# Kernel tuning notes

Hardware: AMD Instinct MI355X
Metric: run time of the kernel (lower is better)

Reference implementation:

```python
import jax, jax.numpy as jnp
import numpy as np

HIDDEN = 1024
INTER = 4096
N_EXPERTS = 8


def geglu(x, w1, w2, w3):
    # x: [N, C], w1/w2: [C, I], w3: [I, C]
    return (jax.nn.gelu(x @ w1, approximate=False) * (x @ w2)) @ w3


def setup_inputs() -> dict:
    key = jax.random.key(0)
    ks = jax.random.split(key, 8)
    s = 0.02
    x = jax.random.normal(ks[0], (2, 2048, HIDDEN), dtype=jnp.float32)
    w1s = jax.random.normal(ks[1], (HIDDEN, INTER), dtype=jnp.float32) * s
    w2s = jax.random.normal(ks[2], (HIDDEN, INTER), dtype=jnp.float32) * s
    w3s = jax.random.normal(ks[3], (INTER, HIDDEN), dtype=jnp.float32) * s
    W1 = jax.random.normal(ks[4], (N_EXPERTS, HIDDEN, INTER), dtype=jnp.float32) * s
    W2 = jax.random.normal(ks[5], (N_EXPERTS, HIDDEN, INTER), dtype=jnp.float32) * s
    W3 = jax.random.normal(ks[6], (N_EXPERTS, INTER, HIDDEN), dtype=jnp.float32) * s
    Wg = jax.random.normal(ks[7], (HIDDEN, N_EXPERTS), dtype=jnp.float32) * s
    return {"x": x, "w1s": w1s, "w2s": w2s, "w3s": w3s,
            "W1": W1, "W2": W2, "W3": W3, "Wg": Wg}


def reference(x, w1s, w2s, w3s, W1, W2, W3, Wg):
    B, T, C = x.shape
    xf = x.reshape(-1, C)  # [N, C]
    shared = geglu(xf, w1s, w2s, w3s)  # [N, C]
    logits = xf @ Wg  # [N, E]
    # top-1 of softmax == argmax of logits (softmax is monotone);
    # NOTE: original torch code does NOT multiply by the routing prob.
    idx = jnp.argmax(logits, axis=-1)  # [N]
    final = jnp.zeros_like(xf)
    for e in range(N_EXPERTS):  # small fixed expert count
        y = geglu(xf, W1[e], W2[e], W3[e])  # [N, C]
        final = final + jnp.where((idx == e)[:, None], y, 0.0)
    return (shared + final).reshape(B, T, C)
```

## Files before the change

### kernel.cpp

```cpp
#include <hip/hip_runtime.h>
#include <stdint.h>

#define HIDDEN 1024
#define INTER  4096
#define NTOK   4096
#define HROWS  (2*NTOK)
#define MAXB   72
#define NMAT   27

typedef unsigned short u16;
typedef unsigned int   u32;
typedef __bf16  bf16x8 __attribute__((ext_vector_type(8)));
typedef float   f32x4  __attribute__((ext_vector_type(4)));
typedef u32     u32x4  __attribute__((ext_vector_type(4)));

#define WAITVM(N) asm volatile("s_waitcnt vmcnt(" #N ")" ::: "memory")

__device__ __forceinline__ void hard_barrier() {
  asm volatile("" ::: "memory");
  __builtin_amdgcn_s_barrier();
  asm volatile("" ::: "memory");
}

__device__ __forceinline__ u16 f2bf(float f) {
  u32 u = __float_as_uint(f);
  u32 r = u + 0x7FFFu + ((u >> 16) & 1u);
  return (u16)(r >> 16);
}

__device__ __forceinline__ u32 cvt_pk_bf16(float lo, float hi) {
  u32 r;
  asm("v_cvt_pk_bf16_f32 %0, %1, %2" : "=v"(r) : "v"(lo), "v"(hi));
  return r;
}

__device__ __forceinline__ void glds16(const void* g, void* l) {
  __builtin_amdgcn_global_load_lds(
      (const __attribute__((address_space(1))) void*)g,
      (__attribute__((address_space(3))) void*)l, 16, 0, 0);
}

__device__ __forceinline__ f32x4 ntload4(const float* p) {
  return __builtin_nontemporal_load((const f32x4*)p);
}

__device__ __forceinline__ int xcd_swz(int orig, int T) {
  int q = T >> 3, r = T & 7;
  int xcd = orig & 7, pos = orig >> 3;
  return (xcd < r ? xcd * (q + 1) : r * (q + 1) + (xcd - r) * q) + pos;
}

__device__ __forceinline__ void blk_entry(const int* cnts, int bx,
                                          int& g, int& hrow0, int& rows, int& pb) {
  if (bx < 32) { g = 8; hrow0 = bx * 128; rows = 128; pb = 0; return; }
  int b = bx - 32, o = 0; g = -1;
  #pragma unroll
  for (int e = 0; e < 8; ++e) {
    int ne = (cnts[e] + 127) >> 7;
    if (g < 0) {
      if (b < ne) {
        g = e; pb = o + b * 128;
        rows = cnts[e] - b * 128; if (rows > 128) rows = 128;
        hrow0 = NTOK + pb;
      } else b -= ne;
    }
    o += cnts[e];
  }
}


__global__ __launch_bounds__(256) void k_pre(
    const float* __restrict__ w1s, const float* __restrict__ w2s,
    const float* __restrict__ w3s, const float* __restrict__ W1,
    const float* __restrict__ W2,  const float* __restrict__ W3,
    u16* __restrict__ Wb,
    const float* __restrict__ x,   const float* __restrict__ wg,
    int* __restrict__ idx, int* __restrict__ cnt, u16* __restrict__ xb)
{
  __shared__ float tileF[32 * 256];
  int tid = threadIdx.x;

  if (blockIdx.x < NMAT * 512) {
    int bid = blockIdx.x;
    int m = bid >> 9, pair = bid & 511;
    const float* src; int N, nkt, kt, pp2;
    if (m < 18) {
      N = INTER; nkt = 32;
      int mm = (m < 9) ? m : m - 9;
      const float* sp = (m < 9) ? w1s : w2s;
      const float* ep = (m < 9) ? W1 : W2;
      src = (mm == 0) ? sp : ep + (size_t)(mm - 1) * HIDDEN * INTER;
      kt = pair >> 4; pp2 = pair & 15;
    } else {
      N = HIDDEN; nkt = 128;
      int mm = m - 18;
      src = (mm == 0) ? w3s : W3 + (size_t)(mm - 1) * INTER * HIDDEN;
      kt = pair >> 2; pp2 = pair & 3;
    }

    const float* in0 = src + (size_t)(kt * 32) * N + pp2 * 256;
    #pragma unroll
    for (int i = 0; i < 8; ++i) {
      int f = tid + 256 * i;
      int k = f >> 6, c4 = f & 63;
      *(f32x4*)&tileF[k * 256 + c4 * 4] = ntload4(in0 + (size_t)k * N + c4 * 4);
    }
    __syncthreads();

    int p2 = tid >> 7, n = tid & 127;
    int pidx = m * 1024 + (pp2 * 2 + p2) * nkt + kt;
    u16* outp = Wb + (size_t)pidx * 4096 + n * 32;
    #pragma unroll
    for (int s = 0; s < 4; ++s) {
      int k8 = s ^ ((n >> 1) & 3);
      const float* col = &tileF[(k8 * 8) * 256 + p2 * 128 + n];
      u32x4 pk;
      pk.x = cvt_pk_bf16(col[0],    col[256]);
      pk.y = cvt_pk_bf16(col[512],  col[768]);
      pk.z = cvt_pk_bf16(col[1024], col[1280]);
      pk.w = cvt_pk_bf16(col[1536], col[1792]);
      *(u32x4*)(outp + s * 8) = pk;
    }
  } else {
    int gb = blockIdx.x - NMAT * 512;
    int wave = tid >> 6, lane = tid & 63;
    int t = gb * 4 + wave;
    if (t >= NTOK) return;
    float acc[8];
    #pragma unroll
    for (int e = 0; e < 8; ++e) acc[e] = 0.f;
    const float* xr = x + (size_t)t * HIDDEN;
    u16* xbr = xb + (size_t)t * HIDDEN;
    #pragma unroll
    for (int it = 0; it < HIDDEN / 4 / 64; ++it) {
      int c4i = it * 64 + lane;
      f32x4 xv = *(const f32x4*)(xr + c4i * 4);
      ushort4 o;
      o.x = f2bf(xv.x); o.y = f2bf(xv.y); o.z = f2bf(xv.z); o.w = f2bf(xv.w);
      *(ushort4*)(xbr + c4i * 4) = o;
      const float* wr = wg + (size_t)c4i * 32;
      #pragma unroll
      for (int u = 0; u < 4; ++u)
        #pragma unroll
        for (int e = 0; e < 8; ++e) acc[e] += xv[u] * wr[u * 8 + e];
    }
    #pragma unroll
    for (int e = 0; e < 8; ++e)
      for (int s = 32; s; s >>= 1) acc[e] += __shfl_xor(acc[e], s);
    if (lane == 0) {
      int best = 0; float bv = acc[0];
      #pragma unroll
      for (int e = 1; e < 8; ++e) if (acc[e] > bv) { bv = acc[e]; best = e; }
      idx[t] = best;
      atomicAdd(&cnt[best], 1);
    }
  }
}

__global__ void k_scatter(const int* __restrict__ idx, const int* __restrict__ cnt,
                          int* __restrict__ fill, int* __restrict__ perm) {
  int t = blockIdx.x * blockDim.x + threadIdx.x;
  if (t >= NTOK) return;
  int e = idx[t];
  int off = 0;
  #pragma unroll
  for (int j = 0; j < 8; ++j) off += (j < e) ? cnt[j] : 0;
  int p = atomicAdd(&fill[e], 1);
  perm[off + p] = t;
}


#define M1_TILE(B, STG, WN)                                                          \
  do {                                                                               \
    const u16* LA = pAr  + (B) * 12288;                                              \
    const u16* L1 = pBr1 + (B) * 12288;                                              \
    const u16* L2 = pBr2 + (B) * 12288;                                              \
    if (STG) {                                                                       \
      char* Ld = smem + (((B) + 2) % 3) * 24576;                                     \
      glds16(srcA0, Ld + w * 2048);                                                  \
      glds16(srcA1, Ld + w * 2048 + 1024);                                           \
      glds16(srcB1, Ld + 8192 + w * 2048);                                           \
      glds16(srcB1 + 1024, Ld + 8192 + w * 2048 + 1024);                             \
      glds16(srcB2, Ld + 16384 + w * 2048);                                          \
      glds16(srcB2 + 1024, Ld + 16384 + w * 2048 + 1024);                            \
      srcA0 += 64; srcA1 += 64; srcB1 += 8192; srcB2 += 8192;                        \
    }                                                                                \
    bf16x8 af[4], b1[4], b2[4];                                                      \
    _Pragma("unroll")                                                                \
    for (int mi = 0; mi < 4; ++mi) af[mi] = *(const bf16x8*)(LA + mi * 512);         \
    _Pragma("unroll")                                                                \
    for (int ni = 0; ni < 4; ++ni) {                                                 \
      b1[ni] = *(const bf16x8*)(L1 + ni * 512);                                      \
      b2[ni] = *(const bf16x8*)(L2 + ni * 512);                                      \
    }                                                                                \
    __builtin_amdgcn_s_setprio(1);                                                   \
    _Pragma("unroll")                                                                \
    for (int mi = 0; mi < 4; ++mi)                                                   \
      _Pragma("unroll")                                                              \
      for (int ni = 0; ni < 4; ++ni) {                                               \
        acc1[mi][ni] = __builtin_amdgcn_mfma_f32_16x16x32_bf16(af[mi], b1[ni], acc1[mi][ni], 0, 0, 0); \
        acc2[mi][ni] = __builtin_amdgcn_mfma_f32_16x16x32_bf16(af[mi], b2[ni], acc2[mi][ni], 0, 0, 0); \
      }                                                                              \
    __builtin_amdgcn_s_setprio(0);                                                   \
    WN;                                                                              \
    hard_barrier();                                                                  \
  } while (0)

__global__ __launch_bounds__(256, 2) void k_mlp1(
    const u16* __restrict__ xb, const u16* __restrict__ Wb,
    const int* __restrict__ perm, const int* __restrict__ cnt,
    u16* __restrict__ Hbuf)
{
  int cnts[8];
  #pragma unroll
  for (int e = 0; e < 8; ++e) cnts[e] = cnt[e];
  int nb = 32;
  #pragma unroll
  for (int e = 0; e < 8; ++e) nb += (cnts[e] + 127) >> 7;
  int T = nb * 32;
  int lid = blockIdx.x;
  if (lid >= T) return;
  int virt = xcd_swz(lid, T);
  int pp = virt / nb;
  int bx = virt - pp * nb;

  int g, hrow0, rows, pb;
  blk_entry(cnts, bx, g, hrow0, rows, pb);
  int m1 = (g == 8) ? 0 : 1 + g;
  int nbase = pp * 128;

  extern __shared__ __align__(16) char smem[];
  int tid = threadIdx.x;
  int w = tid >> 6, lane = tid & 63;
  int q = lane >> 4, rl = lane & 15;
  int mw = w >> 1, nw = w & 1;

  int tokj[2];
  #pragma unroll
  for (int j = 0; j < 2; ++j) {
    int r = w * 32 + j * 16 + (lane >> 2);
    int rc = (r < rows) ? r : (rows - 1);
    tokj[j] = (g == 8) ? (hrow0 + rc) : perm[pb + rc];
  }
  int gch = ((lane & 3) ^ ((lane >> 3) & 3)) * 16;

  const char* srcA0 = (const char*)xb + (size_t)tokj[0] * 2048 + gch;
  const char* srcA1 = (const char*)xb + (size_t)tokj[1] * 2048 + gch;
  const char* srcB1 = (const char*)Wb + ((size_t)m1 * 1024 + pp * 32) * 8192 + w * 2048 + (lane << 4);
  const char* srcB2 = (const char*)Wb + ((size_t)(m1 + 9) * 1024 + pp * 32) * 8192 + w * 2048 + (lane << 4);

  int co = (q ^ ((rl >> 1) & 3)) * 8;
  const u16* pAr  = (const u16*)smem + (mw * 64 + rl) * 32 + co;
  const u16* pBr1 = (const u16*)smem + 4096 + (nw * 64 + rl) * 32 + co;
  const u16* pBr2 = (const u16*)smem + 8192 + (nw * 64 + rl) * 32 + co;

  f32x4 acc1[4][4], acc2[4][4];
  f32x4 z = {0.f, 0.f, 0.f, 0.f};
  #pragma unroll
  for (int mi = 0; mi < 4; ++mi)
    #pragma unroll
    for (int ni = 0; ni < 4; ++ni) { acc1[mi][ni] = z; acc2[mi][ni] = z; }

  #pragma unroll
  for (int p = 0; p < 2; ++p) {
    char* Ld = smem + p * 24576;
    glds16(srcA0, Ld + w * 2048);
    glds16(srcA1, Ld + w * 2048 + 1024);
    glds16(srcB1, Ld + 8192 + w * 2048);
    glds16(srcB1 + 1024, Ld + 8192 + w * 2048 + 1024);
    glds16(srcB2, Ld + 16384 + w * 2048);
    glds16(srcB2 + 1024, Ld + 16384 + w * 2048 + 1024);
    srcA0 += 64; srcA1 += 64; srcB1 += 8192; srcB2 += 8192;
  }
  WAITVM(6);
  hard_barrier();

  for (int r = 0; r < 10; ++r) {
    M1_TILE(0, 1, WAITVM(6));
    M1_TILE(1, 1, WAITVM(6));
    M1_TILE(2, 1, WAITVM(6));
  }
  M1_TILE(0, 0, WAITVM(0));
  M1_TILE(1, 0, (void)0);

  #pragma unroll
  for (int mi = 0; mi < 4; ++mi) {
    #pragma unroll
    for (int j = 0; j < 4; ++j) {
      int r = mw * 64 + mi * 16 + q * 4 + j;
      if (r < rows) {
        size_t hb = (size_t)(hrow0 + r) * INTER + nbase + nw * 64;
        #pragma unroll
        for (int ni = 0; ni < 4; ++ni) {
          float h1 = acc1[mi][ni][j];
          float h2 = acc2[mi][ni][j];
          float ge = 0.5f * h1 * (1.0f + erff(h1 * 0.7071067811865476f));
          __builtin_nontemporal_store(f2bf(ge * h2), &Hbuf[hb + ni * 16 + rl]);
        }
      }
    }
  }
}


#define M2_TILE(B, STG, WN)                                                          \
  do {                                                                               \
    const u16* LA = pAr + (B) * 8192;                                                \
    const u16* LB = pBr + (B) * 8192;                                                \
    if (STG) {                                                                       \
      char* Ld = smem + (((B) + 2) % 3) * 16384;                                     \
      glds16(srcA0, Ld + w * 2048);                                                  \
      glds16(srcA1, Ld + w * 2048 + 1024);                                           \
      glds16(srcB0, Ld + 8192 + w * 2048);                                           \
      glds16(srcB0 + 1024, Ld + 8192 + w * 2048 + 1024);                             \
      srcA0 += 64; srcA1 += 64; srcB0 += 8192;                                       \
    }                                                                                \
    bf16x8 af[4], bf[4];                                                             \
    _Pragma("unroll")                                                                \
    for (int mi = 0; mi < 4; ++mi) af[mi] = *(const bf16x8*)(LA + mi * 512);         \
    _Pragma("unroll")                                                                \
    for (int ni = 0; ni < 4; ++ni) bf[ni] = *(const bf16x8*)(LB + ni * 512);         \
    __builtin_amdgcn_s_setprio(1);                                                   \
    _Pragma("unroll")                                                                \
    for (int mi = 0; mi < 4; ++mi)                                                   \
      _Pragma("unroll")                                                              \
      for (int ni = 0; ni < 4; ++ni)                                                 \
        acc[mi][ni] = __builtin_amdgcn_mfma_f32_16x16x32_bf16(af[mi], bf[ni], acc[mi][ni], 0, 0, 0); \
    __builtin_amdgcn_s_setprio(0);                                                   \
    WN;                                                                              \
    hard_barrier();                                                                  \
  } while (0)

__global__ __launch_bounds__(256, 3) void k_mlp2(
    const u16* __restrict__ Hbuf, const u16* __restrict__ Wb,
    const int* __restrict__ perm, const int* __restrict__ cnt,
    float* __restrict__ out, float* __restrict__ yexp)
{
  int cnts[8];
  #pragma unroll
  for (int e = 0; e < 8; ++e) cnts[e] = cnt[e];
  int nb = 32;
  #pragma unroll
  for (int e = 0; e < 8; ++e) nb += (cnts[e] + 127) >> 7;
  int T = nb * 8;
  int lid = blockIdx.x;
  if (lid >= T) return;
  int virt = xcd_swz(lid, T);
  int pp = virt / nb;
  int bx = virt - pp * nb;

  int g, hrow0, rows, pb;
  blk_entry(cnts, bx, g, hrow0, rows, pb);
  int m3 = (g == 8) ? 18 : 19 + g;
  int nbase = pp * 128;

  extern __shared__ __align__(16) char smem[];
  int tid = threadIdx.x;
  int w = tid >> 6, lane = tid & 63;
  int q = lane >> 4, rl = lane & 15;
  int mw = w >> 1, nw = w & 1;

  int hr[2];
  #pragma unroll
  for (int j = 0; j < 2; ++j) {
    int r = w * 32 + j * 16 + (lane >> 2);
    int rc = (r < rows) ? r : (rows - 1);
    hr[j] = hrow0 + rc;
  }
  int gch = ((lane & 3) ^ ((lane >> 3) & 3)) * 16;

  const char* srcA0 = (const char*)Hbuf + (size_t)hr[0] * (INTER * 2) + gch;
  const char* srcA1 = (const char*)Hbuf + (size_t)hr[1] * (INTER * 2) + gch;
  const char* srcB0 = (const char*)Wb + ((size_t)m3 * 1024 + pp * 128) * 8192 + w * 2048 + (lane << 4);

  int co = (q ^ ((rl >> 1) & 3)) * 8;
  const u16* pAr = (const u16*)smem + (mw * 64 + rl) * 32 + co;
  const u16* pBr = (const u16*)smem + 4096 + (nw * 64 + rl) * 32 + co;

  f32x4 acc[4][4];
  f32x4 z = {0.f, 0.f, 0.f, 0.f};
  #pragma unroll
  for (int mi = 0; mi < 4; ++mi)
    #pragma unroll
    for (int ni = 0; ni < 4; ++ni) acc[mi][ni] = z;

  #pragma unroll
  for (int p = 0; p < 2; ++p) {
    char* Ld = smem + p * 16384;
    glds16(srcA0, Ld + w * 2048);
    glds16(srcA1, Ld + w * 2048 + 1024);
    glds16(srcB0, Ld + 8192 + w * 2048);
    glds16(srcB0 + 1024, Ld + 8192 + w * 2048 + 1024);
    srcA0 += 64; srcA1 += 64; srcB0 += 8192;
  }
  WAITVM(4);
  hard_barrier();

  for (int r = 0; r < 42; ++r) {
    M2_TILE(0, 1, WAITVM(4));
    M2_TILE(1, 1, WAITVM(4));
    M2_TILE(2, 1, WAITVM(4));
  }
  M2_TILE(0, 0, WAITVM(0));
  M2_TILE(1, 0, (void)0);

  float* dstb = (g == 8) ? out : yexp;
  #pragma unroll
  for (int mi = 0; mi < 4; ++mi) {
    #pragma unroll
    for (int j = 0; j < 4; ++j) {
      int r = mw * 64 + mi * 16 + q * 4 + j;
      if (r < rows) {
        int tok = (g == 8) ? (hrow0 + r) : perm[pb + r];
        size_t ob = (size_t)tok * HIDDEN + nbase + nw * 64;
        #pragma unroll
        for (int ni = 0; ni < 4; ++ni)
          __builtin_nontemporal_store(acc[mi][ni][j], &dstb[ob + ni * 16 + rl]);
      }
    }
  }
}

__global__ void k_add(float* __restrict__ out, const float* __restrict__ yexp, int n4) {
  int i = blockIdx.x * blockDim.x + threadIdx.x;
  if (i >= n4) return;
  f32x4 a = __builtin_nontemporal_load(&((const f32x4*)out)[i]);
  f32x4 b = __builtin_nontemporal_load(&((const f32x4*)yexp)[i]);
  a += b;
  ((f32x4*)out)[i] = a;
}


extern "C" void kernel_launch(void* const* d_in, const int* in_sizes, int n_in,
                              void* d_out, int out_size, void* d_ws, size_t ws_size,
                              hipStream_t stream) {
  const float* x   = (const float*)d_in[0];
  const float* w1s = (const float*)d_in[1];
  const float* w2s = (const float*)d_in[2];
  const float* w3s = (const float*)d_in[3];
  const float* W1  = (const float*)d_in[4];
  const float* W2  = (const float*)d_in[5];
  const float* W3  = (const float*)d_in[6];
  const float* Wg  = (const float*)d_in[7];
  float* out = (float*)d_out;

  char* ws = (char*)d_ws;
  size_t o_xb   = 0;
  size_t o_H    = o_xb   + (size_t)NTOK * HIDDEN * 2;
  size_t o_yexp = o_H    + (size_t)HROWS * INTER * 2;
  size_t o_Wb   = o_yexp + (size_t)NTOK * HIDDEN * 4;
  size_t o_idx  = o_Wb   + (size_t)NMAT * 1024 * 8192;
  size_t o_perm = o_idx  + (size_t)NTOK * 4;
  size_t o_cnt  = o_perm + (size_t)NTOK * 4;
  size_t o_fill = o_cnt  + 32;
  size_t need   = o_fill + 32;
  if (ws_size < need) return;

  u16*  xb   = (u16*)(ws + o_xb);
  u16*  Hbuf = (u16*)(ws + o_H);
  float* yexp = (float*)(ws + o_yexp);
  u16*  Wb   = (u16*)(ws + o_Wb);
  int*  idx  = (int*)(ws + o_idx);
  int*  perm = (int*)(ws + o_perm);
  int*  cnt  = (int*)(ws + o_cnt);
  int*  fill = (int*)(ws + o_fill);

  hipMemsetAsync(ws + o_cnt, 0, 64, stream);
  k_pre<<<NMAT * 512 + NTOK / 4, 256, 0, stream>>>(w1s, w2s, w3s, W1, W2, W3, Wb,
                                                   x, Wg, idx, cnt, xb);
  k_scatter<<<NTOK / 256, 256, 0, stream>>>(idx, cnt, fill, perm);
  k_mlp1<<<MAXB * 32, 256, 73728, stream>>>(xb, Wb, perm, cnt, Hbuf);
  k_mlp2<<<MAXB * 8, 256, 49152, stream>>>(Hbuf, Wb, perm, cnt, out, yexp);
  k_add<<<(NTOK * HIDDEN / 4) / 256, 256, 0, stream>>>(out, yexp, NTOK * HIDDEN / 4);
}
```

Before: 473.5 us.

## Fuse shared and expert down-projection into one accumulation, drop k_add and yexp

```diff
diff --git a/kernel.cpp b/kernel.cpp
--- a/kernel.cpp
+++ b/kernel.cpp
@@ -6,6 +6,7 @@
 #define NTOK   4096
 #define HROWS  (2*NTOK)
 #define MAXB   72
+#define MAXB2  40
 #define NMAT   27
 
 typedef unsigned short u16;
@@ -62,6 +63,22 @@
         g = e; pb = o + b * 128;
         rows = cnts[e] - b * 128; if (rows > 128) rows = 128;
         hrow0 = NTOK + pb;
+      } else b -= ne;
+    }
+    o += cnts[e];
+  }
+}
+
+__device__ __forceinline__ void blk_entry_exp(const int* cnts, int bx,
+                                              int& g, int& rows, int& pb) {
+  int b = bx, o = 0; g = -1;
+  #pragma unroll
+  for (int e = 0; e < 8; ++e) {
+    int ne = (cnts[e] + 127) >> 7;
+    if (g < 0) {
+      if (b < ne) {
+        g = e; pb = o + b * 128;
+        rows = cnts[e] - b * 128; if (rows > 128) rows = 128;
       } else b -= ne;
     }
     o += cnts[e];
@@ -334,12 +351,12 @@
 __global__ __launch_bounds__(256, 3) void k_mlp2(
     const u16* __restrict__ Hbuf, const u16* __restrict__ Wb,
     const int* __restrict__ perm, const int* __restrict__ cnt,
-    float* __restrict__ out, float* __restrict__ yexp)
+    float* __restrict__ out)
 {
   int cnts[8];
   #pragma unroll
   for (int e = 0; e < 8; ++e) cnts[e] = cnt[e];
-  int nb = 32;
+  int nb = 0;
   #pragma unroll
   for (int e = 0; e < 8; ++e) nb += (cnts[e] + 127) >> 7;
   int T = nb * 8;
@@ -349,9 +366,8 @@
   int pp = virt / nb;
   int bx = virt - pp * nb;
 
-  int g, hrow0, rows, pb;
-  blk_entry(cnts, bx, g, hrow0, rows, pb);
-  int m3 = (g == 8) ? 18 : 19 + g;
+  int g, rows, pb;
+  blk_entry_exp(cnts, bx, g, rows, pb);
   int nbase = pp * 128;
 
   extern __shared__ __align__(16) char smem[];
@@ -360,18 +376,19 @@
   int q = lane >> 4, rl = lane & 15;
   int mw = w >> 1, nw = w & 1;
 
-  int hr[2];
+  int tokj[2], rcj[2];
   #pragma unroll
   for (int j = 0; j < 2; ++j) {
     int r = w * 32 + j * 16 + (lane >> 2);
     int rc = (r < rows) ? r : (rows - 1);
-    hr[j] = hrow0 + rc;
+    rcj[j] = rc;
+    tokj[j] = perm[pb + rc];
   }
   int gch = ((lane & 3) ^ ((lane >> 3) & 3)) * 16;
 
-  const char* srcA0 = (const char*)Hbuf + (size_t)hr[0] * (INTER * 2) + gch;
-  const char* srcA1 = (const char*)Hbuf + (size_t)hr[1] * (INTER * 2) + gch;
-  const char* srcB0 = (const char*)Wb + ((size_t)m3 * 1024 + pp * 128) * 8192 + w * 2048 + (lane << 4);
+  const char* srcA0 = (const char*)Hbuf + (size_t)tokj[0] * (INTER * 2) + gch;
+  const char* srcA1 = (const char*)Hbuf + (size_t)tokj[1] * (INTER * 2) + gch;
+  const char* srcB0 = (const char*)Wb + ((size_t)18 * 1024 + pp * 128) * 8192 + w * 2048 + (lane << 4);
 
   int co = (q ^ ((rl >> 1) & 3)) * 8;
   const u16* pAr = (const u16*)smem + (mw * 64 + rl) * 32 + co;
@@ -401,33 +418,35 @@
     M2_TILE(1, 1, WAITVM(4));
     M2_TILE(2, 1, WAITVM(4));
   }
-  M2_TILE(0, 0, WAITVM(0));
-  M2_TILE(1, 0, (void)0);
-
-  float* dstb = (g == 8) ? out : yexp;
+
+  srcA0 = (const char*)Hbuf + (size_t)(NTOK + pb + rcj[0]) * (INTER * 2) + gch;
+  srcA1 = (const char*)Hbuf + (size_t)(NTOK + pb + rcj[1]) * (INTER * 2) + gch;
+  srcB0 = (const char*)Wb + ((size_t)(19 + g) * 1024 + pp * 128) * 8192 + w * 2048 + (lane << 4);
+
+  for (int r = 0; r < 42; ++r) {
+    M2_TILE(0, 1, WAITVM(4));
+    M2_TILE(1, 1, WAITVM(4));
+    M2_TILE(2, 1, WAITVM(4));
+  }
+  M2_TILE(0, 1, WAITVM(4));
+  M2_TILE(1, 1, WAITVM(4));
+  M2_TILE(2, 0, WAITVM(0));
+  M2_TILE(0, 0, (void)0);
+
   #pragma unroll
   for (int mi = 0; mi < 4; ++mi) {
     #pragma unroll
     for (int j = 0; j < 4; ++j) {
       int r = mw * 64 + mi * 16 + q * 4 + j;
       if (r < rows) {
-        int tok = (g == 8) ? (hrow0 + r) : perm[pb + r];
+        int tok = perm[pb + r];
         size_t ob = (size_t)tok * HIDDEN + nbase + nw * 64;
         #pragma unroll
         for (int ni = 0; ni < 4; ++ni)
-          __builtin_nontemporal_store(acc[mi][ni][j], &dstb[ob + ni * 16 + rl]);
+          __builtin_nontemporal_store(acc[mi][ni][j], &out[ob + ni * 16 + rl]);
       }
     }
   }
-}
-
-__global__ void k_add(float* __restrict__ out, const float* __restrict__ yexp, int n4) {
-  int i = blockIdx.x * blockDim.x + threadIdx.x;
-  if (i >= n4) return;
-  f32x4 a = __builtin_nontemporal_load(&((const f32x4*)out)[i]);
-  f32x4 b = __builtin_nontemporal_load(&((const f32x4*)yexp)[i]);
-  a += b;
-  ((f32x4*)out)[i] = a;
 }
 
 
@@ -447,8 +466,7 @@
   char* ws = (char*)d_ws;
   size_t o_xb   = 0;
   size_t o_H    = o_xb   + (size_t)NTOK * HIDDEN * 2;
-  size_t o_yexp = o_H    + (size_t)HROWS * INTER * 2;
-  size_t o_Wb   = o_yexp + (size_t)NTOK * HIDDEN * 4;
+  size_t o_Wb   = o_H    + (size_t)HROWS * INTER * 2;
   size_t o_idx  = o_Wb   + (size_t)NMAT * 1024 * 8192;
   size_t o_perm = o_idx  + (size_t)NTOK * 4;
   size_t o_cnt  = o_perm + (size_t)NTOK * 4;
@@ -458,7 +476,6 @@
 
   u16*  xb   = (u16*)(ws + o_xb);
   u16*  Hbuf = (u16*)(ws + o_H);
-  float* yexp = (float*)(ws + o_yexp);
   u16*  Wb   = (u16*)(ws + o_Wb);
   int*  idx  = (int*)(ws + o_idx);
   int*  perm = (int*)(ws + o_perm);
@@ -470,6 +487,5 @@
                                                    x, Wg, idx, cnt, xb);
   k_scatter<<<NTOK / 256, 256, 0, stream>>>(idx, cnt, fill, perm);
   k_mlp1<<<MAXB * 32, 256, 73728, stream>>>(xb, Wb, perm, cnt, Hbuf);
-  k_mlp2<<<MAXB * 8, 256, 49152, stream>>>(Hbuf, Wb, perm, cnt, out, yexp);
-  k_add<<<(NTOK * HIDDEN / 4) / 256, 256, 0, stream>>>(out, yexp, NTOK * HIDDEN / 4);
-}
+  k_mlp2<<<MAXB2 * 8, 256, 49152, stream>>>(Hbuf, Wb, perm, cnt, out);
+}
```

Measured after the change: 497.4 us. +5.0%, slower.
